# Performance work log

Measured on AMD Instinct MI355X. Metric: run time of the kernel, lower is better.

The kernel has to match this reference:

```python
import math
import jax, jax.numpy as jnp
import numpy as np

B, S, E, H = 1, 2048, 2048, 16
QL, KL = 1536, 512          # q_lora_rank, kv_lora_rank
DN, DR, DV = 128, 64, 128   # qk_nope_head_dim, qk_rope_head_dim, v_head_dim
DQ = DN + DR                # q_head_dim = 192
ROPE_BASE = 10000.0
EPS = 1e-6


def _rope_cache(seq_len):
    # YaRN with scaling_factor=1.0 reduces exactly to standard RoPE (freq_extra == freq_inter,
    # mscale ratio == 1), matching DeepseekV2YarnRotaryEmbedding at default settings.
    inv_freq = 1.0 / (ROPE_BASE ** (np.arange(0, DR, 2, dtype=np.float32) / DR))
    t = np.arange(seq_len, dtype=np.float32)
    freqs = np.outer(t, inv_freq)
    emb = np.concatenate([freqs, freqs], axis=-1)  # (S, DR)
    return jnp.asarray(np.cos(emb)), jnp.asarray(np.sin(emb))


def _rmsnorm(x, w):
    return x * jax.lax.rsqrt(jnp.mean(x * x, axis=-1, keepdims=True) + EPS) * w


def _apply_rope(x, cos, sin):
    # x: (B, S, H, D). DeepseekV2 apply_rotary_pos_emb first de-interleaves
    # (view(..., d//2, 2).transpose) then uses rotate_half.
    b, s, h, d = x.shape
    xr = x.reshape(b, s, h, d // 2, 2)
    x = jnp.concatenate([xr[..., 0], xr[..., 1]], axis=-1)  # de-interleave
    rot = jnp.concatenate([-x[..., d // 2:], x[..., : d // 2]], axis=-1)
    return x * cos[None, :, None, :] + rot * sin[None, :, None, :]


def setup_inputs() -> dict:
    key = jax.random.key(0)
    ks = jax.random.split(key, 8)
    w = lambda k, shape, fan_in: (jax.random.normal(k, shape, jnp.float32) / math.sqrt(fan_in))
    return {
        "x": jax.random.normal(ks[0], (B, S, E), jnp.float32),
        "w_q_a": w(ks[1], (E, QL), E),
        "q_a_ln": jnp.ones((QL,), jnp.float32),
        "w_q_b": w(ks[2], (QL, H * DQ), QL),
        "w_kv_a": w(ks[3], (E, KL + DR), E),
        "kv_a_ln": jnp.ones((KL,), jnp.float32),
        "w_kv_b": w(ks[4], (KL, H * (DN + DV)), KL),
        "w_out": w(ks[5], (H * DV, E), H * DV),
    }


def reference(x, w_q_a, q_a_ln, w_q_b, w_kv_a, kv_a_ln, w_kv_b, w_out):
    b, s, _ = x.shape
    # Q: low-rank down-proj -> RMSNorm -> up-proj, split nope/rope parts
    q = (_rmsnorm(x @ w_q_a, q_a_ln) @ w_q_b).reshape(b, s, H, DQ)
    q_nope, q_pe = q[..., :DN], q[..., DN:]
    # KV: joint compressed latent + shared (MQA-style) rope key
    ckv = x @ w_kv_a                         # (b, s, KL+DR)
    c_kv, k_pe = ckv[..., :KL], ckv[..., KL:]
    kv = (_rmsnorm(c_kv, kv_a_ln) @ w_kv_b).reshape(b, s, H, DN + DV)
    k_nope, v = kv[..., :DN], kv[..., DN:]
    # Partial RoPE on the 64-dim rope slice only
    cos, sin = _rope_cache(s)
    q_pe = _apply_rope(q_pe, cos, sin)
    k_pe = _apply_rope(k_pe.reshape(b, s, 1, DR), cos, sin)
    qf = jnp.concatenate([q_nope, q_pe], axis=-1)                       # (b,s,H,192)
    kf = jnp.concatenate([k_nope, jnp.broadcast_to(k_pe, (b, s, H, DR))], axis=-1)
    # Causal softmax attention, scale = 1/sqrt(q_head_dim)
    scale = 1.0 / math.sqrt(DQ)
    scores = jnp.einsum("bqhd,bkhd->bhqk", qf, kf) * scale
    mask = jnp.tril(jnp.ones((s, s), dtype=bool))
    scores = jnp.where(mask[None, None], scores, jnp.finfo(scores.dtype).min)
    p = jax.nn.softmax(scores, axis=-1)
    o = jnp.einsum("bhqk,bkhd->bqhd", p, v).reshape(b, s, H * DV)
    return o @ w_out
```

## Files before the change

kernel.cpp:

```cpp
#include <hip/hip_runtime.h>
#include <hip/hip_bf16.h>
#include <math.h>

#define SS   2048
#define EE   2048
#define HH   16
#define QLAT 1536
#define KLAT 512
#define DN   128
#define DR   64
#define DV   128
#define DQ   192
#define KVD  256
#define CKVW 576
#define QW   3072
#define KVW  4096
#define OW   2048
#define QAC  2112

#define NSEG 4
#define PT_STRIDE 72
#define KTSZ (6 * 64 * 32)

typedef __attribute__((ext_vector_type(8))) short short8;
typedef __attribute__((ext_vector_type(4))) float f32x4;

__global__ void detect_dtype(const unsigned int* __restrict__ lnw, int* flag) {
    *flag = (lnw[0] == 0x3F803F80u) ? 1 : 0;
}

__device__ __forceinline__ float ld_in(const void* p, size_t i, int bf) {
    if (bf) return __bfloat162float(((const __hip_bfloat16*)p)[i]);
    return ((const float*)p)[i];
}

__device__ __forceinline__ ushort f2b(float v) {
    __hip_bfloat16 b = __float2bfloat16(v);
    return *(ushort*)&b;
}
__device__ __forceinline__ float b2f(ushort u) {
    __hip_bfloat16 b = *(__hip_bfloat16*)&u;
    return __bfloat162float(b);
}

__device__ __forceinline__ void async16(const ushort* g, ushort* l) {
    __builtin_amdgcn_global_load_lds(
        (const __attribute__((address_space(1))) void*)g,
        (__attribute__((address_space(3))) void*)l, 16, 0, 0);
}

__global__ __launch_bounds__(256) void conv_x_bf(
    const void* __restrict__ src, ushort* __restrict__ dst, int n, const int* flag) {
    const int bf = *flag;
    int i = (blockIdx.x * 256 + threadIdx.x) * 4;
    if (i >= n) return;
    ushort4 u;
    u.x = f2b(ld_in(src, i + 0, bf));
    u.y = f2b(ld_in(src, i + 1, bf));
    u.z = f2b(ld_in(src, i + 2, bf));
    u.w = f2b(ld_in(src, i + 3, bf));
    *(ushort4*)(dst + i) = u;
}

__global__ __launch_bounds__(256) void transpose5_bf(
    const void* __restrict__ s0, const void* __restrict__ s1,
    const void* __restrict__ s2, const void* __restrict__ s3,
    const void* __restrict__ s4,
    ushort* __restrict__ d0, ushort* __restrict__ d1, ushort* __restrict__ d2,
    ushort* __restrict__ d3, ushort* __restrict__ d4,
    const int* flag) {
    const int z = blockIdx.z;
    const void* in; ushort* out; int R, C;
    switch (z) {
        case 0:  in = s0; out = d0; R = EE;   C = QLAT; break;
        case 1:  in = s1; out = d1; R = EE;   C = CKVW; break;
        case 2:  in = s2; out = d2; R = QLAT; C = QW;   break;
        case 3:  in = s3; out = d3; R = KLAT; C = KVW;  break;
        default: in = s4; out = d4; R = OW;   C = EE;   break;
    }
    const int c0 = blockIdx.x * 64, r0 = blockIdx.y * 64;
    if (c0 >= C || r0 >= R) return;
    const int bf = *flag;
    __shared__ ushort t[64][66];
    const int lane = threadIdx.x & 63, grp = threadIdx.x >> 6;
    #pragma unroll
    for (int p = 0; p < 16; ++p) {
        int r = p * 4 + grp;
        t[lane][r] = f2b(ld_in(in, (size_t)(r0 + r) * C + c0 + lane, bf));
    }
    __syncthreads();
    const int ro = (threadIdx.x & 31) * 2, co = threadIdx.x >> 5;
    #pragma unroll
    for (int p = 0; p < 8; ++p) {
        int c = p * 8 + co;
        ushort2 u = *(const ushort2*)&t[c][ro];
        *(ushort2*)&out[(size_t)(c0 + c) * R + r0 + ro] = u;
    }
}

__global__ __launch_bounds__(256) void gemm_bf(
    const ushort* __restrict__ A, const ushort* __restrict__ Bt,
    void* __restrict__ C, int N, int K, int lda, int ldb, int ldc,
    int cmode, const int* __restrict__ cflag) {
    __shared__ ushort As[2][128 * 32];
    __shared__ ushort Bs[2][128 * 32];
    const int tid = threadIdx.x;
    const int bm = blockIdx.y * 128, bn = blockIdx.x * 128;
    const int lane = tid & 63, wv = tid >> 6;
    const int wm = (wv & 1) * 64, wn = (wv >> 1) * 64;
    const int ln = lane & 15, quad = lane >> 4;

    f32x4 acc[4][4];
    #pragma unroll
    for (int i = 0; i < 4; ++i)
        #pragma unroll
        for (int j = 0; j < 4; ++j) acc[i][j] = (f32x4){0.f, 0.f, 0.f, 0.f};

    const int srow = tid >> 2;
    const int spart = (((tid & 3) ^ ((tid >> 3) & 3))) * 8;
    const ushort* Ag0 = A  + (size_t)(bm + srow) * lda + spart;
    const ushort* Ag1 = Ag0 + (size_t)64 * lda;
    const ushort* Bg0 = Bt + (size_t)(bn + srow) * ldb + spart;
    const ushort* Bg1 = Bg0 + (size_t)64 * ldb;
    const bool bok0 = (bn + srow) < N;
    const bool bok1 = (bn + 64 + srow) < N;
    const int swq = (quad ^ ((ln >> 1) & 3)) * 8;
    const int nsteps = K >> 5;

    {
        ushort* Asl = As[0] + tid * 8;
        ushort* Bsl = Bs[0] + tid * 8;
        async16(Ag0, Asl);
        async16(Ag1, Asl + 2048);
        if (bok0) async16(Bg0, Bsl);
        if (bok1) async16(Bg1, Bsl + 2048);
    }

    for (int c = 0; c < nsteps; ++c) {
        asm volatile("s_waitcnt vmcnt(0)" ::: "memory");
        __builtin_amdgcn_s_barrier();
        asm volatile("" ::: "memory");
        if (c + 1 < nsteps) {
            const int k1 = (c + 1) << 5;
            const int nb = (c + 1) & 1;
            ushort* Asl = As[nb] + tid * 8;
            ushort* Bsl = Bs[nb] + tid * 8;
            async16(Ag0 + k1, Asl);
            async16(Ag1 + k1, Asl + 2048);
            if (bok0) async16(Bg0 + k1, Bsl);
            if (bok1) async16(Bg1 + k1, Bsl + 2048);
        }
        const ushort* Ac = As[c & 1];
        const ushort* Bc = Bs[c & 1];
        short8 af[4], bfr[4];
        #pragma unroll
        for (int t = 0; t < 4; ++t) {
            af[t]  = *(const short8*)&Ac[(wm + t * 16 + ln) * 32 + swq];
            bfr[t] = *(const short8*)&Bc[(wn + t * 16 + ln) * 32 + swq];
        }
        __builtin_amdgcn_s_setprio(1);
        #pragma unroll
        for (int i = 0; i < 4; ++i)
            #pragma unroll
            for (int j = 0; j < 4; ++j)
                acc[i][j] = __builtin_amdgcn_mfma_f32_16x16x32_bf16(af[i], bfr[j], acc[i][j], 0, 0, 0);
        __builtin_amdgcn_s_setprio(0);
    }

    const int cbf = (cmode == 2) ? *cflag : cmode;
    #pragma unroll
    for (int i = 0; i < 4; ++i) {
        #pragma unroll
        for (int r = 0; r < 4; ++r) {
            const int m = bm + wm + i * 16 + quad * 4 + r;
            #pragma unroll
            for (int j = 0; j < 4; ++j) {
                const int n = bn + wn + j * 16 + ln;
                if (n < N) {
                    if (cbf) ((ushort*)C)[(size_t)m * ldc + n] = f2b(acc[i][j][r]);
                    else     ((float*)C)[(size_t)m * ldc + n] = acc[i][j][r];
                }
            }
        }
    }
}

__global__ __launch_bounds__(256) void gemm_bf64(
    const ushort* __restrict__ A, const ushort* __restrict__ Bt,
    void* __restrict__ C, int N, int K, int lda, int ldb, int ldc,
    int cmode, const int* __restrict__ cflag) {
    __shared__ ushort As[2][64 * 32];
    __shared__ ushort Bs[2][128 * 32];
    const int tid = threadIdx.x;
    const int bm = blockIdx.y * 64, bn = blockIdx.x * 128;
    const int lane = tid & 63, wv = tid >> 6;
    const int wm = (wv & 1) * 32, wn = (wv >> 1) * 64;
    const int ln = lane & 15, quad = lane >> 4;

    f32x4 acc[2][4];
    #pragma unroll
    for (int i = 0; i < 2; ++i)
        #pragma unroll
        for (int j = 0; j < 4; ++j) acc[i][j] = (f32x4){0.f, 0.f, 0.f, 0.f};

    const int srow = tid >> 2;
    const int spart = (((tid & 3) ^ ((tid >> 3) & 3))) * 8;
    const ushort* Ag0 = A  + (size_t)(bm + srow) * lda + spart;
    const ushort* Bg0 = Bt + (size_t)(bn + srow) * ldb + spart;
    const ushort* Bg1 = Bg0 + (size_t)64 * ldb;
    const bool bok0 = (bn + srow) < N;
    const bool bok1 = (bn + 64 + srow) < N;
    const int swq = (quad ^ ((ln >> 1) & 3)) * 8;
    const int nsteps = K >> 5;

    {
        ushort* Asl = As[0] + tid * 8;
        ushort* Bsl = Bs[0] + tid * 8;
        async16(Ag0, Asl);
        if (bok0) async16(Bg0, Bsl);
        if (bok1) async16(Bg1, Bsl + 2048);
    }

    for (int c = 0; c < nsteps; ++c) {
        asm volatile("s_waitcnt vmcnt(0)" ::: "memory");
        __builtin_amdgcn_s_barrier();
        asm volatile("" ::: "memory");
        if (c + 1 < nsteps) {
            const int k1 = (c + 1) << 5;
            const int nb = (c + 1) & 1;
            ushort* Asl = As[nb] + tid * 8;
            ushort* Bsl = Bs[nb] + tid * 8;
            async16(Ag0 + k1, Asl);
            if (bok0) async16(Bg0 + k1, Bsl);
            if (bok1) async16(Bg1 + k1, Bsl + 2048);
        }
        const ushort* Ac = As[c & 1];
        const ushort* Bc = Bs[c & 1];
        short8 af[2], bfr[4];
        #pragma unroll
        for (int t = 0; t < 2; ++t)
            af[t] = *(const short8*)&Ac[(wm + t * 16 + ln) * 32 + swq];
        #pragma unroll
        for (int t = 0; t < 4; ++t)
            bfr[t] = *(const short8*)&Bc[(wn + t * 16 + ln) * 32 + swq];
        __builtin_amdgcn_s_setprio(1);
        #pragma unroll
        for (int i = 0; i < 2; ++i)
            #pragma unroll
            for (int j = 0; j < 4; ++j)
                acc[i][j] = __builtin_amdgcn_mfma_f32_16x16x32_bf16(af[i], bfr[j], acc[i][j], 0, 0, 0);
        __builtin_amdgcn_s_setprio(0);
    }

    const int cbf = (cmode == 2) ? *cflag : cmode;
    #pragma unroll
    for (int i = 0; i < 2; ++i) {
        #pragma unroll
        for (int r = 0; r < 4; ++r) {
            const int m = bm + wm + i * 16 + quad * 4 + r;
            #pragma unroll
            for (int j = 0; j < 4; ++j) {
                const int n = bn + wn + j * 16 + ln;
                if (n < N) {
                    if (cbf) ((ushort*)C)[(size_t)m * ldc + n] = f2b(acc[i][j][r]);
                    else     ((float*)C)[(size_t)m * ldc + n] = acc[i][j][r];
                }
            }
        }
    }
}

__global__ __launch_bounds__(256) void rmsnorm2_bf(
    ushort* __restrict__ x, const void* __restrict__ wq,
    const void* __restrict__ wkv, const int* wflag) {
    const int wbf = *wflag;
    const int which = blockIdx.y;
    const int cols = which ? KLAT : QLAT;
    const void* w = which ? wkv : wq;
    ushort* p = x + (size_t)blockIdx.x * QAC + (which ? QLAT : 0);
    float ss = 0.f;
    for (int i = threadIdx.x; i < cols; i += 256) { float v = b2f(p[i]); ss += v * v; }
    #pragma unroll
    for (int off = 32; off; off >>= 1) ss += __shfl_xor(ss, off);
    __shared__ float red[4];
    const int wid = threadIdx.x >> 6, lane = threadIdx.x & 63;
    if (lane == 0) red[wid] = ss;
    __syncthreads();
    const float tot = red[0] + red[1] + red[2] + red[3];
    const float scale = rsqrtf(tot / (float)cols + 1e-6f);
    for (int i = threadIdx.x; i < cols; i += 256)
        p[i] = f2b(b2f(p[i]) * scale * ld_in(w, i, wbf));
}

__global__ __launch_bounds__(256) void rope_tab(float* __restrict__ tab) {
    int idx = blockIdx.x * 256 + threadIdx.x;
    int s = idx >> 5, i = idx & 31;
    float inv = powf(10000.0f, -(float)i / 32.0f);
    float sv, cv;
    sincosf((float)s * inv, &sv, &cv);
    tab[idx * 2]     = cv;
    tab[idx * 2 + 1] = sv;
}

__device__ __forceinline__ void rope_block(
    const ushort* __restrict__ src, ushort* __restrict__ dst,
    const float* __restrict__ tb) {
    short8 vin[8];
    #pragma unroll
    for (int t = 0; t < 8; ++t) vin[t] = *(const short8*)(src + t * 8);
    short8 lo[4], hi[4];
    #pragma unroll
    for (int t = 0; t < 4; ++t) {
        #pragma unroll
        for (int j = 0; j < 8; ++j) {
            const int i = t * 8 + j;
            float cv = tb[2 * i], sv = tb[2 * i + 1];
            ushort u0 = ((const ushort*)&vin[(2 * i) >> 3])[(2 * i) & 7];
            ushort u1 = ((const ushort*)&vin[(2 * i + 1) >> 3])[(2 * i + 1) & 7];
            float x0 = b2f(u0), x1 = b2f(u1);
            lo[t][j] = (short)f2b(x0 * cv - x1 * sv);
            hi[t][j] = (short)f2b(x1 * cv + x0 * sv);
        }
    }
    #pragma unroll
    for (int t = 0; t < 4; ++t) {
        *(short8*)(dst + t * 8)      = lo[t];
        *(short8*)(dst + 32 + t * 8) = hi[t];
    }
}

__global__ __launch_bounds__(256) void rope_apply(
    ushort* __restrict__ q, const ushort* __restrict__ qac,
    ushort* __restrict__ kpe, const float* __restrict__ tab) {
    int idx = blockIdx.x * blockDim.x + threadIdx.x;
    if (idx < SS * HH) {
        int s = idx >> 4, h = idx & 15;
        ushort* p = q + (size_t)s * QW + h * DQ + DN;
        rope_block(p, p, tab + s * 64);
    } else if (idx < SS * HH + SS) {
        int s = idx - SS * HH;
        rope_block(qac + (size_t)s * QAC + QLAT + KLAT,
                   kpe + (size_t)s * DR, tab + s * 64);
    }
}

__global__ __launch_bounds__(256) void build_kf(
    const ushort* __restrict__ kv, const ushort* __restrict__ kpe,
    ushort* __restrict__ kf) {
    int idx = blockIdx.x * 256 + threadIdx.x;
    int part = idx % 24;
    int rest = idx / 24;
    int h = rest & 15, s = rest >> 4;
    short8 v;
    if (part < 16) v = *(const short8*)(kv + (size_t)s * KVW + h * KVD + part * 8);
    else           v = *(const short8*)(kpe + (size_t)s * DR + (part - 16) * 8);
    *(short8*)(kf + ((size_t)h * SS + s) * 192 + part * 8) = v;
}

__global__ __launch_bounds__(256) void build_vt2(
    const ushort* __restrict__ kv, ushort* __restrict__ vt2) {
    __shared__ ushort Vl[64 * 136];
    const int ck = blockIdx.x, h = blockIdx.y;
    const int tid = threadIdx.x;
    const int lane = tid & 63, wv = tid >> 6;
    #pragma unroll
    for (int rr = 0; rr < 4; ++rr) {
        int n = rr * 256 + tid;
        int key = n >> 4, part = n & 15;
        short8 v = *(const short8*)(kv + (size_t)(ck * 64 + key) * KVW + h * KVD + DN + part * 8);
        *(short8*)&Vl[key * 136 + part * 8] = v;
    }
    __syncthreads();
    const int ln = lane & 15, quad = lane >> 4;
    ushort* dst = vt2 + (((size_t)h * 32 + ck) * 16) * 512;
    #pragma unroll
    for (int w = 0; w < 4; ++w) {
        int idx2 = wv * 4 + w;
        int kb2 = idx2 >> 3, nb = idx2 & 7;
        short8 v;
        #pragma unroll
        for (int j = 0; j < 8; ++j)
            ((ushort*)&v)[j] = Vl[(kb2 * 32 + quad * 8 + j) * 136 + nb * 16 + ln];
        *(short8*)(dst + (size_t)idx2 * 512 + lane * 8) = v;
    }
}

__global__ __launch_bounds__(256, 2) void attn_mfma2(
    const ushort* __restrict__ qbf, const ushort* __restrict__ kf,
    const ushort* __restrict__ vt2, ushort* __restrict__ opart,
    float* __restrict__ ml) {
    const int seg = blockIdx.x, bq = 31 - blockIdx.y, h = blockIdx.z;
    const int ctot = bq + 1;
    const int c_lo = (seg * ctot) >> 2;
    const int nch = (((seg + 1) * ctot) >> 2) - c_lo;
    if (nch <= 0) return;

    __shared__ ushort Kt[2 * KTSZ];
    __shared__ ushort Pt[4][16 * PT_STRIDE];

    const int tid = threadIdx.x, lane = tid & 63, wl = tid >> 6;
    const int ln = lane & 15, quad = lane >> 4;
    const int qw = bq * 64 + wl * 16;
    const int kstart = c_lo << 6;
    const float scale = 0.07216878364870322f;

    short8 aq[6];
    const ushort* qrow = qbf + (size_t)(qw + ln) * QW + h * DQ;
    #pragma unroll
    for (int kb = 0; kb < 6; ++kb)
        aq[kb] = *(const short8*)(qrow + kb * 32 + quad * 8);

    const ushort* kfh = kf + (size_t)h * SS * 192;
    const ushort* vth2 = vt2 + ((size_t)h * 32 * 16) * 512 + lane * 8;

    const int key_s = tid >> 2;
    const int swp = ((tid & 3) ^ ((tid >> 3) & 3)) * 8;
    const ushort* kg = kfh + (size_t)(kstart + key_s) * 192 + swp;
    const int swq = (quad ^ ((ln >> 1) & 3)) * 8;

    f32x4 oacc[8];
    #pragma unroll
    for (int f = 0; f < 8; ++f) oacc[f] = (f32x4){0.f, 0.f, 0.f, 0.f};
    float mrow[4] = {-INFINITY, -INFINITY, -INFINITY, -INFINITY};
    float lrow[4] = {0.f, 0.f, 0.f, 0.f};

    {
        ushort* kd = Kt + tid * 8;
        #pragma unroll
        for (int i = 0; i < 6; ++i)
            async16(kg + i * 32, kd + i * 2048);
        kg += (size_t)64 * 192;
    }

    for (int c = 0; c < nch; ++c) {
        const int k0 = kstart + (c << 6);
        asm volatile("s_waitcnt vmcnt(0)" ::: "memory");
        __builtin_amdgcn_s_barrier();
        asm volatile("" ::: "memory");
        if (c + 1 < nch) {
            ushort* kd = Kt + ((c + 1) & 1) * KTSZ + tid * 8;
            #pragma unroll
            for (int i = 0; i < 6; ++i)
                async16(kg + i * 32, kd + i * 2048);
            kg += (size_t)64 * 192;
        }
        const ushort* Kcur = Kt + (c & 1) * KTSZ;

        const ushort* vfr = vth2 + (size_t)(k0 >> 6) * 16 * 512;
        short8 bv0[8];
        #pragma unroll
        for (int nb = 0; nb < 8; ++nb)
            bv0[nb] = *(const short8*)(vfr + (size_t)nb * 512);
        f32x4 s[4];
        #pragma unroll
        for (int ns = 0; ns < 4; ++ns) s[ns] = (f32x4){0.f, 0.f, 0.f, 0.f};
        __builtin_amdgcn_s_setprio(1);
        #pragma unroll
        for (int ns = 0; ns < 4; ++ns)
            #pragma unroll
            for (int kb = 0; kb < 6; ++kb) {
                short8 bk = *(const short8*)&Kcur[(kb * 64 + ns * 16 + ln) * 32 + swq];
                s[ns] = __builtin_amdgcn_mfma_f32_16x16x32_bf16(aq[kb], bk, s[ns], 0, 0, 0);
            }
        __builtin_amdgcn_s_setprio(0);
        float pv[4][4], rmax[4];
        #pragma unroll
        for (int r = 0; r < 4; ++r) rmax[r] = -1e30f;
        #pragma unroll
        for (int ns = 0; ns < 4; ++ns)
            #pragma unroll
            for (int r = 0; r < 4; ++r) {
                int key = k0 + ns * 16 + ln;
                int qr = qw + quad * 4 + r;
                float v = s[ns][r] * scale;
                if (key > qr) v = -1e30f;
                pv[ns][r] = v;
                rmax[r] = fmaxf(rmax[r], v);
            }
        #pragma unroll
        for (int off = 8; off; off >>= 1)
            #pragma unroll
            for (int r = 0; r < 4; ++r)
                rmax[r] = fmaxf(rmax[r], __shfl_xor(rmax[r], off));
        float alpha[4], psum[4];
        #pragma unroll
        for (int r = 0; r < 4; ++r) {
            float mnew = fmaxf(mrow[r], rmax[r]);
            alpha[r] = __expf(mrow[r] - mnew);
            mrow[r] = mnew;
        }
        #pragma unroll
        for (int ns = 0; ns < 4; ++ns)
            #pragma unroll
            for (int r = 0; r < 4; ++r)
                pv[ns][r] = __expf(pv[ns][r] - mrow[r]);
        #pragma unroll
        for (int r = 0; r < 4; ++r)
            psum[r] = (pv[0][r] + pv[1][r]) + (pv[2][r] + pv[3][r]);
        #pragma unroll
        for (int off = 8; off; off >>= 1)
            #pragma unroll
            for (int r = 0; r < 4; ++r)
                psum[r] += __shfl_xor(psum[r], off);
        #pragma unroll
        for (int r = 0; r < 4; ++r) lrow[r] = lrow[r] * alpha[r] + psum[r];
        #pragma unroll
        for (int f = 0; f < 8; ++f)
            #pragma unroll
            for (int r = 0; r < 4; ++r) oacc[f][r] *= alpha[r];
        #pragma unroll
        for (int ns = 0; ns < 4; ++ns)
            #pragma unroll
            for (int r = 0; r < 4; ++r)
                Pt[wl][(quad * 4 + r) * PT_STRIDE + ns * 16 + ln] = f2b(pv[ns][r]);
        short8 bv1[8];
        #pragma unroll
        for (int nb = 0; nb < 8; ++nb)
            bv1[nb] = *(const short8*)(vfr + (size_t)(8 + nb) * 512);
        short8 pa0 = *(const short8*)&Pt[wl][ln * PT_STRIDE + quad * 8];
        short8 pa1 = *(const short8*)&Pt[wl][ln * PT_STRIDE + 32 + quad * 8];
        __builtin_amdgcn_s_setprio(1);
        #pragma unroll
        for (int nb = 0; nb < 8; ++nb)
            oacc[nb] = __builtin_amdgcn_mfma_f32_16x16x32_bf16(pa0, bv0[nb], oacc[nb], 0, 0, 0);
        #pragma unroll
        for (int nb = 0; nb < 8; ++nb)
            oacc[nb] = __builtin_amdgcn_mfma_f32_16x16x32_bf16(pa1, bv1[nb], oacc[nb], 0, 0, 0);
        __builtin_amdgcn_s_setprio(0);
    }

    const size_t pbase = (((size_t)h * 32 + bq) * NSEG + seg) * 64;
    #pragma unroll
    for (int nb = 0; nb < 8; ++nb)
        #pragma unroll
        for (int r = 0; r < 4; ++r)
            opart[(pbase + wl * 16 + quad * 4 + r) * 128 + nb * 16 + ln] = f2b(oacc[nb][r]);
    if (ln == 0) {
        #pragma unroll
        for (int r = 0; r < 4; ++r) {
            ml[(pbase + wl * 16 + quad * 4 + r) * 2]     = mrow[r];
            ml[(pbase + wl * 16 + quad * 4 + r) * 2 + 1] = lrow[r];
        }
    }
}

__global__ __launch_bounds__(256) void merge_attn(
    const ushort* __restrict__ opart, const float* __restrict__ ml,
    ushort* __restrict__ obf) {
    const int q = blockIdx.x;
    const int bq = q >> 6, row = q & 63;
    const int ctot = bq + 1;
    const int t = threadIdx.x;
    #pragma unroll
    for (int pp = 0; pp < 8; ++pp) {
        int idx = pp * 256 + t;
        int h = idx >> 7, d = idx & 127;
        size_t rbase = (((size_t)h * 32 + bq) * NSEG) * 64 + row;
        float M = -1e30f;
        #pragma unroll
        for (int s = 0; s < NSEG; ++s) {
            if ((((s + 1) * ctot) >> 2) > ((s * ctot) >> 2))
                M = fmaxf(M, ml[(rbase + (size_t)s * 64) * 2]);
        }
        float L = 0.f, acc = 0.f;
        #pragma unroll
        for (int s = 0; s < NSEG; ++s) {
            if ((((s + 1) * ctot) >> 2) > ((s * ctot) >> 2)) {
                size_t ri = rbase + (size_t)s * 64;
                float w = __expf(ml[ri * 2] - M);
                L += w * ml[ri * 2 + 1];
                acc += w * b2f(opart[ri * 128 + d]);
            }
        }
        obf[(size_t)q * OW + h * DV + d] = f2b(acc / L);
    }
}

extern "C" void kernel_launch(void* const* d_in, const int* in_sizes, int n_in,
                              void* d_out, int out_size, void* d_ws, size_t ws_size,
                              hipStream_t stream) {
    const void* x       = d_in[0];
    const void* w_q_a   = d_in[1];
    const void* q_a_ln  = d_in[2];
    const void* w_q_b   = d_in[3];
    const void* w_kv_a  = d_in[4];
    const void* kv_a_ln = d_in[5];
    const void* w_kv_b  = d_in[6];
    const void* w_out   = d_in[7];

    char* ws = (char*)d_ws;
    int*    flag  = (int*)ws;
    ushort* qbf   = (ushort*)(ws + 256);
    ushort* obf   = qbf   + (size_t)SS * QW;
    ushort* wqat  = obf   + (size_t)SS * OW;
    ushort* wkvat = wqat  + (size_t)QLAT * EE;
    ushort* wqbt  = wkvat + (size_t)CKVW * EE;
    ushort* wkvbt = wqbt  + (size_t)QW * QLAT;
    ushort* woutt = wkvbt + (size_t)KVW * KLAT;
    ushort* kf    = woutt + (size_t)EE * OW;
    ushort* vt2   = kf    + (size_t)HH * SS * 192;
    float*  ml    = (float*)(vt2 + (size_t)HH * SS * DV);
    ushort* qac   = (ushort*)(ml + (size_t)HH * 32 * NSEG * 64 * 2);
    ushort* xbf   = qac   + (size_t)SS * QAC;
    ushort* kvbf  = xbf   + (size_t)SS * EE;
    ushort* kpebf = kvbf  + (size_t)SS * KVW;
    float*  rtab  = (float*)(kpebf + (size_t)SS * DR);
    ushort* opart = qac;

    detect_dtype<<<1, 1, 0, stream>>>((const unsigned int*)q_a_ln, flag);
    rope_tab<<<SS * 32 / 256, 256, 0, stream>>>(rtab);

    conv_x_bf<<<(SS * EE / 4 + 255) / 256, 256, 0, stream>>>(x, xbf, SS * EE, flag);
    transpose5_bf<<<dim3(64, 32, 5), 256, 0, stream>>>(
        w_q_a, w_kv_a, w_q_b, w_kv_b, w_out,
        wqat, wkvat, wqbt, wkvbt, woutt, flag);

    gemm_bf64<<<dim3((QAC + 127) / 128, SS / 64), 256, 0, stream>>>(
        xbf, wqat, qac, QAC, EE, EE, EE, QAC, 1, nullptr);

    rmsnorm2_bf<<<dim3(SS, 2), 256, 0, stream>>>(qac, q_a_ln, kv_a_ln, flag);

    gemm_bf<<<dim3(QW / 128, SS / 128), 256, 0, stream>>>(
        qac, wqbt, qbf, QW, QLAT, QAC, QLAT, QW, 1, nullptr);
    gemm_bf<<<dim3(KVW / 128, SS / 128), 256, 0, stream>>>(
        qac + QLAT, wkvbt, kvbf, KVW, KLAT, QAC, KLAT, KVW, 1, nullptr);

    rope_apply<<<(SS * HH + SS + 255) / 256, 256, 0, stream>>>(qbf, qac, kpebf, rtab);

    build_kf<<<SS * HH * 24 / 256, 256, 0, stream>>>(kvbf, kpebf, kf);
    build_vt2<<<dim3(SS / 64, HH), 256, 0, stream>>>(kvbf, vt2);

    attn_mfma2<<<dim3(NSEG, SS / 64, HH), 256, 0, stream>>>(qbf, kf, vt2, opart, ml);
    merge_attn<<<SS, 256, 0, stream>>>(opart, ml, obf);

    gemm_bf64<<<dim3(EE / 128, SS / 64), 256, 0, stream>>>(
        obf, woutt, d_out, EE, OW, OW, OW, EE, 2, flag);
}
```

Measured before the change: 410.3 us.

## Merge Q/KV up-projection GEMMs, fuse rope/kf/vt2 kernels, deepen GEMM K-tile

The two up-projection GEMMs now run as one launch that picks Q or KV work by blockIdx.z, so both can occupy the GPU together. Rope on q, building kf (with the k_pe rope done inline) and building vt2 are merged into a single kernel, which drops the kpebf intermediate and several launches. Both GEMM kernels now load K-tiles of 64 instead of 32 with an 8-way XOR swizzle and clamp out-of-range B rows rather than using per-row predicates, which halves the barriers per K but doubles shared memory per block. The merged GEMM grid launches idle blocks for the narrower Q part, and the larger LDS footprint may lower occupancy.

Result: faster. 372.2 us (-9.3%).

```diff
diff --git a/kernel.cpp b/kernel.cpp
--- a/kernel.cpp
+++ b/kernel.cpp
@@ -98,14 +98,11 @@
     }
 }
 
-__global__ __launch_bounds__(256) void gemm_bf(
+__device__ __forceinline__ void gemm128_body(
     const ushort* __restrict__ A, const ushort* __restrict__ Bt,
     void* __restrict__ C, int N, int K, int lda, int ldb, int ldc,
-    int cmode, const int* __restrict__ cflag) {
-    __shared__ ushort As[2][128 * 32];
-    __shared__ ushort Bs[2][128 * 32];
+    int cbf, int bm, int bn, ushort* As, ushort* Bs) {
     const int tid = threadIdx.x;
-    const int bm = blockIdx.y * 128, bn = blockIdx.x * 128;
     const int lane = tid & 63, wv = tid >> 6;
     const int wm = (wv & 1) * 64, wn = (wv >> 1) * 64;
     const int ln = lane & 15, quad = lane >> 4;
@@ -116,58 +113,67 @@
         #pragma unroll
         for (int j = 0; j < 4; ++j) acc[i][j] = (f32x4){0.f, 0.f, 0.f, 0.f};
 
-    const int srow = tid >> 2;
-    const int spart = (((tid & 3) ^ ((tid >> 3) & 3))) * 8;
-    const ushort* Ag0 = A  + (size_t)(bm + srow) * lda + spart;
-    const ushort* Ag1 = Ag0 + (size_t)64 * lda;
-    const ushort* Bg0 = Bt + (size_t)(bn + srow) * ldb + spart;
-    const ushort* Bg1 = Bg0 + (size_t)64 * ldb;
-    const bool bok0 = (bn + srow) < N;
-    const bool bok1 = (bn + 64 + srow) < N;
-    const int swq = (quad ^ ((ln >> 1) & 3)) * 8;
-    const int nsteps = K >> 5;
+    const int srow = tid >> 3;
+    const int spart = ((tid & 7) ^ ((tid >> 3) & 7)) * 8;
+    const ushort* Ag0 = A + (size_t)(bm + srow) * lda + spart;
+    const ushort* Ag1 = Ag0 + (size_t)32 * lda;
+    const ushort* Ag2 = Ag0 + (size_t)64 * lda;
+    const ushort* Ag3 = Ag0 + (size_t)96 * lda;
+    const int br0 = (bn + srow)      < N ? (bn + srow)      : (N - 1);
+    const int br1 = (bn + 32 + srow) < N ? (bn + 32 + srow) : (N - 1);
+    const int br2 = (bn + 64 + srow) < N ? (bn + 64 + srow) : (N - 1);
+    const int br3 = (bn + 96 + srow) < N ? (bn + 96 + srow) : (N - 1);
+    const ushort* Bg0 = Bt + (size_t)br0 * ldb + spart;
+    const ushort* Bg1 = Bt + (size_t)br1 * ldb + spart;
+    const ushort* Bg2 = Bt + (size_t)br2 * ldb + spart;
+    const ushort* Bg3 = Bt + (size_t)br3 * ldb + spart;
+    const int nsteps = K >> 6;
 
     {
-        ushort* Asl = As[0] + tid * 8;
-        ushort* Bsl = Bs[0] + tid * 8;
-        async16(Ag0, Asl);
-        async16(Ag1, Asl + 2048);
-        if (bok0) async16(Bg0, Bsl);
-        if (bok1) async16(Bg1, Bsl + 2048);
-    }
-
+        ushort* as = As + tid * 8;
+        ushort* bs = Bs + tid * 8;
+        async16(Ag0, as);          async16(Ag1, as + 2048);
+        async16(Ag2, as + 4096);   async16(Ag3, as + 6144);
+        async16(Bg0, bs);          async16(Bg1, bs + 2048);
+        async16(Bg2, bs + 4096);   async16(Bg3, bs + 6144);
+    }
+
+    int cb = 0;
     for (int c = 0; c < nsteps; ++c) {
         asm volatile("s_waitcnt vmcnt(0)" ::: "memory");
         __builtin_amdgcn_s_barrier();
         asm volatile("" ::: "memory");
         if (c + 1 < nsteps) {
-            const int k1 = (c + 1) << 5;
-            const int nb = (c + 1) & 1;
-            ushort* Asl = As[nb] + tid * 8;
-            ushort* Bsl = Bs[nb] + tid * 8;
-            async16(Ag0 + k1, Asl);
-            async16(Ag1 + k1, Asl + 2048);
-            if (bok0) async16(Bg0 + k1, Bsl);
-            if (bok1) async16(Bg1 + k1, Bsl + 2048);
-        }
-        const ushort* Ac = As[c & 1];
-        const ushort* Bc = Bs[c & 1];
-        short8 af[4], bfr[4];
-        #pragma unroll
-        for (int t = 0; t < 4; ++t) {
-            af[t]  = *(const short8*)&Ac[(wm + t * 16 + ln) * 32 + swq];
-            bfr[t] = *(const short8*)&Bc[(wn + t * 16 + ln) * 32 + swq];
-        }
-        __builtin_amdgcn_s_setprio(1);
-        #pragma unroll
-        for (int i = 0; i < 4; ++i)
-            #pragma unroll
-            for (int j = 0; j < 4; ++j)
-                acc[i][j] = __builtin_amdgcn_mfma_f32_16x16x32_bf16(af[i], bfr[j], acc[i][j], 0, 0, 0);
-        __builtin_amdgcn_s_setprio(0);
-    }
-
-    const int cbf = (cmode == 2) ? *cflag : cmode;
+            const int k1 = (c + 1) << 6;
+            ushort* as = As + (cb ^ 1) * 8192 + tid * 8;
+            ushort* bs = Bs + (cb ^ 1) * 8192 + tid * 8;
+            async16(Ag0 + k1, as);          async16(Ag1 + k1, as + 2048);
+            async16(Ag2 + k1, as + 4096);   async16(Ag3 + k1, as + 6144);
+            async16(Bg0 + k1, bs);          async16(Bg1 + k1, bs + 2048);
+            async16(Bg2 + k1, bs + 4096);   async16(Bg3 + k1, bs + 6144);
+        }
+        const ushort* Ac = As + cb * 8192;
+        const ushort* Bc = Bs + cb * 8192;
+        #pragma unroll
+        for (int ks = 0; ks < 2; ++ks) {
+            const int sw = ((ks * 4 + quad) ^ (ln & 7)) * 8;
+            short8 af[4], bfr[4];
+            #pragma unroll
+            for (int t = 0; t < 4; ++t) {
+                af[t]  = *(const short8*)&Ac[(wm + t * 16 + ln) * 64 + sw];
+                bfr[t] = *(const short8*)&Bc[(wn + t * 16 + ln) * 64 + sw];
+            }
+            __builtin_amdgcn_s_setprio(1);
+            #pragma unroll
+            for (int i = 0; i < 4; ++i)
+                #pragma unroll
+                for (int j = 0; j < 4; ++j)
+                    acc[i][j] = __builtin_amdgcn_mfma_f32_16x16x32_bf16(af[i], bfr[j], acc[i][j], 0, 0, 0);
+            __builtin_amdgcn_s_setprio(0);
+        }
+        cb ^= 1;
+    }
+
     #pragma unroll
     for (int i = 0; i < 4; ++i) {
         #pragma unroll
@@ -185,74 +191,101 @@
     }
 }
 
+__global__ __launch_bounds__(256) void gemm_qkv(
+    const ushort* __restrict__ qac, const ushort* __restrict__ wqbt,
+    const ushort* __restrict__ wkvbt, ushort* __restrict__ qbf_,
+    ushort* __restrict__ kvbf_) {
+    __shared__ ushort As[2 * 8192];
+    __shared__ ushort Bs[2 * 8192];
+    if (blockIdx.z == 0) {
+        if (blockIdx.x >= QW / 128) return;
+        gemm128_body(qac, wqbt, qbf_, QW, QLAT, QAC, QLAT, QW, 1,
+                     blockIdx.y * 128, blockIdx.x * 128, As, Bs);
+    } else {
+        gemm128_body(qac + QLAT, wkvbt, kvbf_, KVW, KLAT, QAC, KLAT, KVW, 1,
+                     blockIdx.y * 128, blockIdx.x * 128, As, Bs);
+    }
+}
+
 __global__ __launch_bounds__(256) void gemm_bf64(
     const ushort* __restrict__ A, const ushort* __restrict__ Bt,
     void* __restrict__ C, int N, int K, int lda, int ldb, int ldc,
     int cmode, const int* __restrict__ cflag) {
-    __shared__ ushort As[2][64 * 32];
-    __shared__ ushort Bs[2][128 * 32];
+    __shared__ ushort As[2 * 4096];
+    __shared__ ushort Bs[2 * 8192];
     const int tid = threadIdx.x;
     const int bm = blockIdx.y * 64, bn = blockIdx.x * 128;
     const int lane = tid & 63, wv = tid >> 6;
     const int wm = (wv & 1) * 32, wn = (wv >> 1) * 64;
     const int ln = lane & 15, quad = lane >> 4;
 
+    int cbf = cmode;
+    if (cmode == 2) cbf = *(volatile const int*)cflag;
+
     f32x4 acc[2][4];
     #pragma unroll
     for (int i = 0; i < 2; ++i)
         #pragma unroll
         for (int j = 0; j < 4; ++j) acc[i][j] = (f32x4){0.f, 0.f, 0.f, 0.f};
 
-    const int srow = tid >> 2;
-    const int spart = (((tid & 3) ^ ((tid >> 3) & 3))) * 8;
-    const ushort* Ag0 = A  + (size_t)(bm + srow) * lda + spart;
-    const ushort* Bg0 = Bt + (size_t)(bn + srow) * ldb + spart;
-    const ushort* Bg1 = Bg0 + (size_t)64 * ldb;
-    const bool bok0 = (bn + srow) < N;
-    const bool bok1 = (bn + 64 + srow) < N;
-    const int swq = (quad ^ ((ln >> 1) & 3)) * 8;
-    const int nsteps = K >> 5;
+    const int srow = tid >> 3;
+    const int spart = ((tid & 7) ^ ((tid >> 3) & 7)) * 8;
+    const ushort* Ag0 = A + (size_t)(bm + srow) * lda + spart;
+    const ushort* Ag1 = Ag0 + (size_t)32 * lda;
+    const int br0 = (bn + srow)      < N ? (bn + srow)      : (N - 1);
+    const int br1 = (bn + 32 + srow) < N ? (bn + 32 + srow) : (N - 1);
+    const int br2 = (bn + 64 + srow) < N ? (bn + 64 + srow) : (N - 1);
+    const int br3 = (bn + 96 + srow) < N ? (bn + 96 + srow) : (N - 1);
+    const ushort* Bg0 = Bt + (size_t)br0 * ldb + spart;
+    const ushort* Bg1 = Bt + (size_t)br1 * ldb + spart;
+    const ushort* Bg2 = Bt + (size_t)br2 * ldb + spart;
+    const ushort* Bg3 = Bt + (size_t)br3 * ldb + spart;
+    const int nsteps = K >> 6;
 
     {
-        ushort* Asl = As[0] + tid * 8;
-        ushort* Bsl = Bs[0] + tid * 8;
-        async16(Ag0, Asl);
-        if (bok0) async16(Bg0, Bsl);
-        if (bok1) async16(Bg1, Bsl + 2048);
-    }
-
+        ushort* as = As + tid * 8;
+        ushort* bs = Bs + tid * 8;
+        async16(Ag0, as);          async16(Ag1, as + 2048);
+        async16(Bg0, bs);          async16(Bg1, bs + 2048);
+        async16(Bg2, bs + 4096);   async16(Bg3, bs + 6144);
+    }
+
+    int cb = 0;
     for (int c = 0; c < nsteps; ++c) {
         asm volatile("s_waitcnt vmcnt(0)" ::: "memory");
         __builtin_amdgcn_s_barrier();
         asm volatile("" ::: "memory");
         if (c + 1 < nsteps) {
-            const int k1 = (c + 1) << 5;
-            const int nb = (c + 1) & 1;
-            ushort* Asl = As[nb] + tid * 8;
-            ushort* Bsl = Bs[nb] + tid * 8;
-            async16(Ag0 + k1, Asl);
-            if (bok0) async16(Bg0 + k1, Bsl);
-            if (bok1) async16(Bg1 + k1, Bsl + 2048);
-        }
-        const ushort* Ac = As[c & 1];
-        const ushort* Bc = Bs[c & 1];
-        short8 af[2], bfr[4];
-        #pragma unroll
-        for (int t = 0; t < 2; ++t)
-            af[t] = *(const short8*)&Ac[(wm + t * 16 + ln) * 32 + swq];
-        #pragma unroll
-        for (int t = 0; t < 4; ++t)
-            bfr[t] = *(const short8*)&Bc[(wn + t * 16 + ln) * 32 + swq];
-        __builtin_amdgcn_s_setprio(1);
-        #pragma unroll
-        for (int i = 0; i < 2; ++i)
-            #pragma unroll
-            for (int j = 0; j < 4; ++j)
-                acc[i][j] = __builtin_amdgcn_mfma_f32_16x16x32_bf16(af[i], bfr[j], acc[i][j], 0, 0, 0);
-        __builtin_amdgcn_s_setprio(0);
-    }
-
-    const int cbf = (cmode == 2) ? *cflag : cmode;
+            const int k1 = (c + 1) << 6;
+            ushort* as = As + (cb ^ 1) * 4096 + tid * 8;
+            ushort* bs = Bs + (cb ^ 1) * 8192 + tid * 8;
+            async16(Ag0 + k1, as);          async16(Ag1 + k1, as + 2048);
+            async16(Bg0 + k1, bs);          async16(Bg1 + k1, bs + 2048);
+            async16(Bg2 + k1, bs + 4096);   async16(Bg3 + k1, bs + 6144);
+        }
+        const ushort* Ac = As + cb * 4096;
+        const ushort* Bc = Bs + cb * 8192;
+        #pragma unroll
+        for (int ks = 0; ks < 2; ++ks) {
+            const int sw = ((ks * 4 + quad) ^ (ln & 7)) * 8;
+            short8 af[2], bfr[4];
+            #pragma unroll
+            for (int t = 0; t < 2; ++t)
+                af[t] = *(const short8*)&Ac[(wm + t * 16 + ln) * 64 + sw];
+            #pragma unroll
+            for (int t = 0; t < 4; ++t)
+                bfr[t] = *(const short8*)&Bc[(wn + t * 16 + ln) * 64 + sw];
+            __builtin_amdgcn_s_setprio(1);
+            #pragma unroll
+            for (int i = 0; i < 2; ++i)
+                #pragma unroll
+                for (int j = 0; j < 4; ++j)
+                    acc[i][j] = __builtin_amdgcn_mfma_f32_16x16x32_bf16(af[i], bfr[j], acc[i][j], 0, 0, 0);
+            __builtin_amdgcn_s_setprio(0);
+        }
+        cb ^= 1;
+    }
+
     #pragma unroll
     for (int i = 0; i < 2; ++i) {
         #pragma unroll
@@ -329,59 +362,68 @@
     }
 }
 
-__global__ __launch_bounds__(256) void rope_apply(
+__global__ __launch_bounds__(256) void fuse3(
     ushort* __restrict__ q, const ushort* __restrict__ qac,
-    ushort* __restrict__ kpe, const float* __restrict__ tab) {
-    int idx = blockIdx.x * blockDim.x + threadIdx.x;
-    if (idx < SS * HH) {
+    const ushort* __restrict__ kv, ushort* __restrict__ kf,
+    ushort* __restrict__ vt2, const float* __restrict__ tab) {
+    __shared__ ushort Vl[64 * 136];
+    const int b = blockIdx.x;
+    const int tid = threadIdx.x;
+    if (b < 128) {
+        int idx = b * 256 + tid;
         int s = idx >> 4, h = idx & 15;
         ushort* p = q + (size_t)s * QW + h * DQ + DN;
         rope_block(p, p, tab + s * 64);
-    } else if (idx < SS * HH + SS) {
-        int s = idx - SS * HH;
-        rope_block(qac + (size_t)s * QAC + QLAT + KLAT,
-                   kpe + (size_t)s * DR, tab + s * 64);
-    }
-}
-
-__global__ __launch_bounds__(256) void build_kf(
-    const ushort* __restrict__ kv, const ushort* __restrict__ kpe,
-    ushort* __restrict__ kf) {
-    int idx = blockIdx.x * 256 + threadIdx.x;
-    int part = idx % 24;
-    int rest = idx / 24;
-    int h = rest & 15, s = rest >> 4;
-    short8 v;
-    if (part < 16) v = *(const short8*)(kv + (size_t)s * KVW + h * KVD + part * 8);
-    else           v = *(const short8*)(kpe + (size_t)s * DR + (part - 16) * 8);
-    *(short8*)(kf + ((size_t)h * SS + s) * 192 + part * 8) = v;
-}
-
-__global__ __launch_bounds__(256) void build_vt2(
-    const ushort* __restrict__ kv, ushort* __restrict__ vt2) {
-    __shared__ ushort Vl[64 * 136];
-    const int ck = blockIdx.x, h = blockIdx.y;
-    const int tid = threadIdx.x;
-    const int lane = tid & 63, wv = tid >> 6;
-    #pragma unroll
-    for (int rr = 0; rr < 4; ++rr) {
-        int n = rr * 256 + tid;
-        int key = n >> 4, part = n & 15;
-        short8 v = *(const short8*)(kv + (size_t)(ck * 64 + key) * KVW + h * KVD + DN + part * 8);
-        *(short8*)&Vl[key * 136 + part * 8] = v;
-    }
-    __syncthreads();
-    const int ln = lane & 15, quad = lane >> 4;
-    ushort* dst = vt2 + (((size_t)h * 32 + ck) * 16) * 512;
-    #pragma unroll
-    for (int w = 0; w < 4; ++w) {
-        int idx2 = wv * 4 + w;
-        int kb2 = idx2 >> 3, nb = idx2 & 7;
+    } else if (b < 128 + 3072) {
+        int idx = (b - 128) * 256 + tid;
+        int part = idx % 24;
+        int rest = idx / 24;
+        int h = rest & 15, s = rest >> 4;
         short8 v;
-        #pragma unroll
-        for (int j = 0; j < 8; ++j)
-            ((ushort*)&v)[j] = Vl[(kb2 * 32 + quad * 8 + j) * 136 + nb * 16 + ln];
-        *(short8*)(dst + (size_t)idx2 * 512 + lane * 8) = v;
+        if (part < 16) {
+            v = *(const short8*)(kv + (size_t)s * KVW + h * KVD + part * 8);
+        } else {
+            const int j8 = part - 16;
+            const int seg = j8 & 3;
+            const ushort* cp = qac + (size_t)s * QAC + QLAT + KLAT + seg * 16;
+            short8 a = *(const short8*)cp;
+            short8 bb = *(const short8*)(cp + 8);
+            const float* tb = tab + s * 64 + seg * 16;
+            const bool hi = (j8 >= 4);
+            #pragma unroll
+            for (int jj = 0; jj < 8; ++jj) {
+                float cv = tb[2 * jj], sv = tb[2 * jj + 1];
+                ushort u0 = (jj < 4) ? (ushort)a[2 * jj]     : (ushort)bb[2 * jj - 8];
+                ushort u1 = (jj < 4) ? (ushort)a[2 * jj + 1] : (ushort)bb[2 * jj - 7];
+                float x0 = b2f(u0), x1 = b2f(u1);
+                v[jj] = (short)f2b(hi ? (x1 * cv + x0 * sv) : (x0 * cv - x1 * sv));
+            }
+        }
+        *(short8*)(kf + ((size_t)h * SS + s) * 192 + part * 8) = v;
+    } else {
+        const int r = b - (128 + 3072);
+        const int ck = r & 31, h = r >> 5;
+        const int lane = tid & 63, wv = tid >> 6;
+        #pragma unroll
+        for (int rr = 0; rr < 4; ++rr) {
+            int n = rr * 256 + tid;
+            int key = n >> 4, part = n & 15;
+            short8 v = *(const short8*)(kv + (size_t)(ck * 64 + key) * KVW + h * KVD + DN + part * 8);
+            *(short8*)&Vl[key * 136 + part * 8] = v;
+        }
+        __syncthreads();
+        const int ln = lane & 15, quad = lane >> 4;
+        ushort* dst = vt2 + (((size_t)h * 32 + ck) * 16) * 512;
+        #pragma unroll
+        for (int w = 0; w < 4; ++w) {
+            int idx2 = wv * 4 + w;
+            int kb2 = idx2 >> 3, nb = idx2 & 7;
+            short8 v;
+            #pragma unroll
+            for (int j = 0; j < 8; ++j)
+                ((ushort*)&v)[j] = Vl[(kb2 * 32 + quad * 8 + j) * 136 + nb * 16 + ln];
+            *(short8*)(dst + (size_t)idx2 * 512 + lane * 8) = v;
+        }
     }
 }
 
@@ -620,15 +662,10 @@
 
     rmsnorm2_bf<<<dim3(SS, 2), 256, 0, stream>>>(qac, q_a_ln, kv_a_ln, flag);
 
-    gemm_bf<<<dim3(QW / 128, SS / 128), 256, 0, stream>>>(
-        qac, wqbt, qbf, QW, QLAT, QAC, QLAT, QW, 1, nullptr);
-    gemm_bf<<<dim3(KVW / 128, SS / 128), 256, 0, stream>>>(
-        qac + QLAT, wkvbt, kvbf, KVW, KLAT, QAC, KLAT, KVW, 1, nullptr);
-
-    rope_apply<<<(SS * HH + SS + 255) / 256, 256, 0, stream>>>(qbf, qac, kpebf, rtab);
-
-    build_kf<<<SS * HH * 24 / 256, 256, 0, stream>>>(kvbf, kpebf, kf);
-    build_vt2<<<dim3(SS / 64, HH), 256, 0, stream>>>(kvbf, vt2);
+    gemm_qkv<<<dim3(KVW / 128, SS / 128, 2), 256, 0, stream>>>(
+        qac, wqbt, wkvbt, qbf, kvbf);
+
+    fuse3<<<128 + 3072 + 512, 256, 0, stream>>>(qbf, qac, kvbf, kf, vt2, rtab);
 
     attn_mfma2<<<dim3(NSEG, SS / 64, HH), 256, 0, stream>>>(qbf, kf, vt2, opart, ml);
     merge_attn<<<SS, 256, 0, stream>>>(opart, ml, obf);
```
